# Kernel optimization log

Measured on AMD Instinct MI355X. Metric: run time of the kernel, lower is better.

Reference implementation:

```python
import jax, jax.numpy as jnp
import numpy as np

N_LOC = 20000
N_EXP = 200000
H = 64
E = 1500000
L = 400000


def setup_inputs() -> dict:
    key = jax.random.key(0)
    ks = jax.random.split(key, 24)
    f = jnp.float32
    w = lambda k, shp: jax.random.normal(k, shp, dtype=f) * 0.1
    # edges: ('location','of','experts'): src in [0,N_LOC), dst in [0,N_EXP)
    src = jax.random.randint(ks[0], (E,), 0, N_LOC)
    dst = jax.random.randint(ks[1], (E,), 0, N_EXP)
    edge_of = jnp.stack([src, dst])          # location -> experts
    edge_rev = jnp.stack([dst, src])         # experts -> location (ToUndirected)
    row = jax.random.randint(ks[2], (L,), 0, N_LOC)
    col = jax.random.randint(ks[3], (L,), 0, N_EXP)
    edge_label_index = jnp.stack([row, col])
    return dict(
        emb_loc=w(ks[4], (N_LOC, H)), emb_exp=w(ks[5], (N_EXP, H)),
        W1l_of=w(ks[6], (H, H)), b1_of=jnp.zeros((H,), f), W1r_of=w(ks[7], (H, H)),
        W1l_rev=w(ks[8], (H, H)), b1_rev=jnp.zeros((H,), f), W1r_rev=w(ks[9], (H, H)),
        W2l_of=w(ks[10], (H, H)), b2_of=jnp.zeros((H,), f), W2r_of=w(ks[11], (H, H)),
        W2l_rev=w(ks[12], (H, H)), b2_rev=jnp.zeros((H,), f), W2r_rev=w(ks[13], (H, H)),
        dW1=w(ks[14], (2 * H, H)), db1=jnp.zeros((H,), f),
        dW2=w(ks[15], (H, 1)), db2=jnp.zeros((1,), f),
        edge_of=edge_of, edge_rev=edge_rev, edge_label_index=edge_label_index,
    )


def _sage(x_src, x_dst, edge, Wl, b, Wr, n_dst):
    # PyG SAGEConv: lin_l(mean of neighbor msgs) + lin_r(x_dst); bias only in lin_l
    s, d = edge[0], edge[1]
    msg = x_src[s]                                   # [E, H] gather
    summed = jax.ops.segment_sum(msg, d, num_segments=n_dst)
    cnt = jax.ops.segment_sum(jnp.ones((edge.shape[1],), x_src.dtype), d, num_segments=n_dst)
    agg = summed / jnp.maximum(cnt, 1.0)[:, None]
    return agg @ Wl + b + x_dst @ Wr


def reference(emb_loc, emb_exp,
              W1l_of, b1_of, W1r_of, W1l_rev, b1_rev, W1r_rev,
              W2l_of, b2_of, W2r_of, W2l_rev, b2_rev, W2r_rev,
              dW1, db1, dW2, db2,
              edge_of, edge_rev, edge_label_index):
    # layer 1 (to_hetero: one conv per edge type; each dst type has one incoming type)
    z_exp = jax.nn.relu(_sage(emb_loc, emb_exp, edge_of, W1l_of, b1_of, W1r_of, N_EXP))
    z_loc = jax.nn.relu(_sage(emb_exp, emb_loc, edge_rev, W1l_rev, b1_rev, W1r_rev, N_LOC))
    # layer 2 (no relu)
    z_exp2 = _sage(z_loc, z_exp, edge_of, W2l_of, b2_of, W2r_of, N_EXP)
    z_loc2 = _sage(z_exp, z_loc, edge_rev, W2l_rev, b2_rev, W2r_rev, N_LOC)
    # EdgeDecoder: gather-concat-MLP
    row, col = edge_label_index[0], edge_label_index[1]
    z = jnp.concatenate([z_loc2[row], z_exp2[col]], axis=-1)  # [L, 2H]
    h = jax.nn.relu(z @ dW1 + db1)
    out = (h @ dW2 + db2).reshape(-1)
    return out
```

## Files before the change

### kernel.cpp

```cpp
#include <hip/hip_runtime.h>

#define H 64
#define NE 1500000
#define NLOC 20000
#define NEXP 200000
#define NL 400000
#define PAD_E 32
#define PAD_L 128
#define EPT 8
#define FILL_CHUNK 2048

#define WS_NEED 90480000ULL

typedef int vint4 __attribute__((ext_vector_type(4)));
typedef _Float16 f16x8 __attribute__((ext_vector_type(8)));
typedef float f32x4 __attribute__((ext_vector_type(4)));

__device__ __forceinline__ float bcastf(float v, int k) {
  return __int_as_float(__builtin_amdgcn_readlane(__float_as_int(v), k));
}
__device__ __forceinline__ int bcasti(int v, int k) {
  return __builtin_amdgcn_readlane(v, k);
}

__global__ __launch_bounds__(256) void fill_kernel(
    const int* __restrict__ src, const int* __restrict__ dst,
    int* __restrict__ cnt_loc, int* __restrict__ cnt_exp,
    int* __restrict__ nbr_loc, unsigned short* __restrict__ nbr_exp)
{
  const int p = blockIdx.x & 7;
  const int chunk = blockIdx.x >> 3;
  const long base = (long)chunk * FILL_CHUNK + threadIdx.x * EPT;
  if (base >= NE) return;
  vint4 s0 = *(const vint4*)(src + base);
  vint4 s1 = *(const vint4*)(src + base + 4);
  vint4 d0 = *(const vint4*)(dst + base);
  vint4 d1 = *(const vint4*)(dst + base + 4);
  int ss[EPT] = {s0.x, s0.y, s0.z, s0.w, s1.x, s1.y, s1.z, s1.w};
  int dd[EPT] = {d0.x, d0.y, d0.z, d0.w, d1.x, d1.y, d1.z, d1.w};
  const int elo = p * (NEXP / 8), ehi = elo + NEXP / 8;
  const int llo = p * (NLOC / 8), lhi = llo + NLOC / 8;
#pragma unroll
  for (int k = 0; k < EPT; k++) {
    const int d = dd[k];
    if (d >= elo && d < ehi) {
      int pos = atomicAdd(&cnt_exp[d], 1);
      if (pos < PAD_E) nbr_exp[d * PAD_E + pos] = (unsigned short)ss[k];
    }
  }
#pragma unroll
  for (int k = 0; k < EPT; k++) {
    const int s = ss[k];
    if (s >= llo && s < lhi) {
      int pos = atomicAdd(&cnt_loc[s], 1);
      if (pos < PAD_L) nbr_loc[s * PAD_L + pos] = dd[k];
    }
  }
}

__global__ __launch_bounds__(256, 4) void dense_linear_kernel(
    const float* __restrict__ x, _Float16* __restrict__ out16,
    float* __restrict__ out32, const float* __restrict__ W, int n)
{
  const int lane = threadIdx.x & 63;
  const int gw = (blockIdx.x * 256 + threadIdx.x) >> 6;
  const int nw = (gridDim.x * 256) >> 6;
  float w[H];
#pragma unroll
  for (int k = 0; k < H; k++) w[k] = W[k * H + lane];
  for (int i = gw; i < n; i += nw) {
    const float xv = x[i * H + lane];
    float a0 = 0.f, a1 = 0.f;
#pragma unroll
    for (int k = 0; k < H; k += 2) {
      a0 += bcastf(xv, k)     * w[k];
      a1 += bcastf(xv, k + 1) * w[k + 1];
    }
    if (out16) out16[i * H + lane] = (_Float16)(a0 + a1);
    else       out32[i * H + lane] = a0 + a1;
  }
}

__global__ __launch_bounds__(256, 4) void mfma_pass_kernel(
    const unsigned short* __restrict__ nbr, const int* __restrict__ cnt,
    const _Float16* __restrict__ y,
    const float* a32, const _Float16* a16,
    _Float16* out1, const float* __restrict__ W1,
    const float* __restrict__ bias, int relu,
    _Float16* out2, const float* __restrict__ W2)
{
  const int w = threadIdx.x >> 6;
  const int lane = threadIdx.x & 63;
  const int q = lane >> 4;
  const int cidx = lane & 15;
  const int rb = blockIdx.x * 16;

  __shared__ float Gs[16 * H];

  f16x8 b1lo, b1hi, b2lo, b2hi;
#pragma unroll
  for (int j = 0; j < 8; j++) {
    b1lo[j] = (_Float16)W1[(q * 8 + j) * H + w * 16 + cidx];
    b1hi[j] = (_Float16)W1[(32 + q * 8 + j) * H + w * 16 + cidx];
  }
  if (out2) {
#pragma unroll
    for (int j = 0; j < 8; j++) {
      b2lo[j] = (_Float16)W2[(q * 8 + j) * H + w * 16 + cidx];
      b2hi[j] = (_Float16)W2[(32 + q * 8 + j) * H + w * 16 + cidx];
    }
  }

  if (y) {
    for (int rr = 0; rr < 4; rr++) {
      const int i = rb + w * 4 + rr;
      const int c = cnt[i];
      const int cc = min(c, PAD_E);
      const unsigned short* nb = nbr + (long)i * PAD_E;
      float s0 = 0.f, s1 = 0.f, s2 = 0.f, s3 = 0.f;
      const int id = (lane < cc) ? (int)nb[lane] : 0;
      int k = 0;
      const int m4 = cc & ~3;
      for (; k < m4; k += 4) {
        const int i0 = bcasti(id, k), i1 = bcasti(id, k + 1),
                  i2 = bcasti(id, k + 2), i3 = bcasti(id, k + 3);
        s0 += (float)y[(long)i0 * H + lane];
        s1 += (float)y[(long)i1 * H + lane];
        s2 += (float)y[(long)i2 * H + lane];
        s3 += (float)y[(long)i3 * H + lane];
      }
      for (; k < cc; k++) s0 += (float)y[(long)bcasti(id, k) * H + lane];
      Gs[(w * 4 + rr) * H + lane] =
          ((s0 + s1) + (s2 + s3)) / fmaxf((float)c, 1.0f);
    }
  }

  f16x8 a0, a1;
  if (a16) {
    const _Float16* ar = a16 + (long)(rb + cidx) * H;
    a0 = *(const f16x8*)(ar + q * 8);
    a1 = *(const f16x8*)(ar + 32 + q * 8);
  } else {
    const float* ar = a32 + (long)(rb + cidx) * H;
#pragma unroll
    for (int j = 0; j < 8; j++) {
      a0[j] = (_Float16)ar[q * 8 + j];
      a1[j] = (_Float16)ar[32 + q * 8 + j];
    }
  }
  f32x4 acc1 = {0.f, 0.f, 0.f, 0.f};
  acc1 = __builtin_amdgcn_mfma_f32_16x16x32_f16(a0, b1lo, acc1, 0, 0, 0);
  acc1 = __builtin_amdgcn_mfma_f32_16x16x32_f16(a1, b1hi, acc1, 0, 0, 0);
  f32x4 acc2 = {0.f, 0.f, 0.f, 0.f};
  if (out2) {
    acc2 = __builtin_amdgcn_mfma_f32_16x16x32_f16(a0, b2lo, acc2, 0, 0, 0);
    acc2 = __builtin_amdgcn_mfma_f32_16x16x32_f16(a1, b2hi, acc2, 0, 0, 0);
  }

  const float bj = bias ? bias[w * 16 + cidx] : 0.f;
  __syncthreads();
#pragma unroll
  for (int reg = 0; reg < 4; reg++) {
    const int r = q * 4 + reg;
    float v = acc1[reg] + bj;
    if (y) v += Gs[r * H + w * 16 + cidx];
    if (relu) v = fmaxf(v, 0.f);
    out1[(long)(rb + r) * H + w * 16 + cidx] = (_Float16)v;
    if (out2)
      out2[(long)(rb + r) * H + w * 16 + cidx] = (_Float16)acc2[reg];
  }
}

__global__ __launch_bounds__(256, 4) void loc_gather_kernel(
    const int* __restrict__ nbr, const int* __restrict__ cnt,
    const _Float16* __restrict__ T, const float* __restrict__ x,
    float* __restrict__ out, const float* __restrict__ Wr,
    const float* __restrict__ bias, int n, int relu)
{
  const int lane = threadIdx.x & 63;
  const int gw = (blockIdx.x * 256 + threadIdx.x) >> 6;
  const int nw = (gridDim.x * 256) >> 6;
  float wr[H];
#pragma unroll
  for (int k = 0; k < H; k++) wr[k] = Wr[k * H + lane];
  const float bj = bias[lane];
  for (int i = gw; i < n; i += nw) {
    const int c = cnt[i];
    const int cc = min(c, PAD_L);
    const int* nb = nbr + (long)i * PAD_L;
    float s0 = 0.f, s1 = 0.f, s2 = 0.f, s3 = 0.f;
    int e = 0;
    while (e < cc) {
      const int m = min(cc - e, 64);
      const int id = (lane < m) ? nb[e + lane] : 0;
      int k = 0;
      const int m4 = m & ~3;
      for (; k < m4; k += 4) {
        const int i0 = bcasti(id, k), i1 = bcasti(id, k + 1),
                  i2 = bcasti(id, k + 2), i3 = bcasti(id, k + 3);
        s0 += (float)T[(long)i0 * H + lane];
        s1 += (float)T[(long)i1 * H + lane];
        s2 += (float)T[(long)i2 * H + lane];
        s3 += (float)T[(long)i3 * H + lane];
      }
      for (; k < m; k++) s0 += (float)T[(long)bcasti(id, k) * H + lane];
      e += m;
    }
    const float agg = ((s0 + s1) + (s2 + s3)) / fmaxf((float)c, 1.0f);
    const float xv = x[i * H + lane];
    float a0 = 0.f, a1 = 0.f;
#pragma unroll
    for (int k = 0; k < H; k += 2) {
      a0 += bcastf(xv, k)     * wr[k];
      a1 += bcastf(xv, k + 1) * wr[k + 1];
    }
    float acc = agg + bj + a0 + a1;
    if (relu) acc = fmaxf(acc, 0.0f);
    out[i * H + lane] = acc;
  }
}

__global__ __launch_bounds__(256, 4) void edge_kernel(
    const int* __restrict__ row, const int* __restrict__ col,
    const float* __restrict__ P, const _Float16* __restrict__ Q,
    const float* __restrict__ db1, const float* __restrict__ dW2,
    const float* __restrict__ db2, float* __restrict__ out)
{
  const int lane = threadIdx.x & 63;
  const int gw = (blockIdx.x * 256 + threadIdx.x) >> 6;
  const int nw = (gridDim.x * 256) >> 6;
  const float bj = db1[lane];
  const float w2 = dW2[lane];
  const float b2 = db2[0];
  for (int e = gw * 2; e < NL; e += nw * 2) {
    const int r0 = row[e],     c0 = col[e];
    const int r1 = row[e + 1], c1 = col[e + 1];
    const float p0 = P[(long)r0 * H + lane];
    const float q0 = (float)Q[(long)c0 * H + lane];
    const float p1 = P[(long)r1 * H + lane];
    const float q1 = (float)Q[(long)c1 * H + lane];
    float h0 = fmaxf(p0 + q0 + bj, 0.0f) * w2;
    float h1 = fmaxf(p1 + q1 + bj, 0.0f) * w2;
#pragma unroll
    for (int off = 1; off < 64; off <<= 1) {
      h0 += __shfl_xor(h0, off);
      h1 += __shfl_xor(h1, off);
    }
    if (lane == 0) {
      out[e]     = h0 + b2;
      out[e + 1] = h1 + b2;
    }
  }
}

extern "C" void kernel_launch(void* const* d_in, const int* in_sizes, int n_in,
                              void* d_out, int out_size, void* d_ws, size_t ws_size,
                              hipStream_t stream) {
  const float* emb_loc = (const float*)d_in[0];
  const float* emb_exp = (const float*)d_in[1];
  const float* W1l_of  = (const float*)d_in[2];
  const float* b1_of   = (const float*)d_in[3];
  const float* W1r_of  = (const float*)d_in[4];
  const float* W1l_rev = (const float*)d_in[5];
  const float* b1_rev  = (const float*)d_in[6];
  const float* W1r_rev = (const float*)d_in[7];
  const float* W2l_of  = (const float*)d_in[8];
  const float* b2_of   = (const float*)d_in[9];
  const float* W2r_of  = (const float*)d_in[10];
  const float* W2l_rev = (const float*)d_in[11];
  const float* b2_rev  = (const float*)d_in[12];
  const float* W2r_rev = (const float*)d_in[13];
  const float* dW1     = (const float*)d_in[14];
  const float* db1     = (const float*)d_in[15];
  const float* dW2     = (const float*)d_in[16];
  const float* db2     = (const float*)d_in[17];
  const int*   edge_of = (const int*)d_in[18];
  const int*   eli     = (const int*)d_in[20];

  const int* src = edge_of;
  const int* dst = edge_of + NE;
  const int* row = eli;
  const int* col = eli + NL;

  if (ws_size < WS_NEED) return;

  char* ws = (char*)d_ws;
  int*            cnt_loc = (int*)(ws);
  int*            cnt_exp = (int*)(ws + 80000);
  int*            nbr_loc = (int*)(ws + 880000);
  unsigned short* nbr_exp = (unsigned short*)(ws + 11120000);
  _Float16*       Ylh     = (_Float16*)(ws + 23920000);
  _Float16*       Y2lh    = (_Float16*)(ws + 26480000);
  float*          z_loc   = (float*)(ws + 29040000);
  float*          z_loc2  = (float*)(ws + 34160000);
  _Float16*       ZE      = (_Float16*)(ws + 39280000);
  _Float16*       TH      = (_Float16*)(ws + 64880000);
  float*          out     = (float*)d_out;

  (void)hipMemsetAsync(ws, 0, 880000, stream);
  const int chunks = (NE + FILL_CHUNK - 1) / FILL_CHUNK;
  fill_kernel<<<chunks * 8, 256, 0, stream>>>(src, dst, cnt_loc, cnt_exp,
                                              nbr_loc, nbr_exp);

  dense_linear_kernel<<<1280, 256, 0, stream>>>(emb_loc, Ylh, nullptr,
                                                W1l_of, NLOC);
  mfma_pass_kernel<<<NEXP / 16, 256, 0, stream>>>(nbr_exp, cnt_exp, Ylh,
      emb_exp, (const _Float16*)nullptr, ZE, W1r_of, b1_of, 1, TH, W1l_rev);
  loc_gather_kernel<<<1250, 256, 0, stream>>>(nbr_loc, cnt_loc, TH,
      emb_loc, z_loc, W1r_rev, b1_rev, NLOC, 1);

  dense_linear_kernel<<<1280, 256, 0, stream>>>(z_loc, Y2lh, nullptr,
                                                W2l_of, NLOC);
  mfma_pass_kernel<<<NEXP / 16, 256, 0, stream>>>(nbr_exp, cnt_exp, Y2lh,
      (const float*)nullptr, ZE, ZE, W2r_of, b2_of, 0, TH, W2l_rev);
  loc_gather_kernel<<<1250, 256, 0, stream>>>(nbr_loc, cnt_loc, TH,
      z_loc, z_loc2, W2r_rev, b2_rev, NLOC, 0);

  dense_linear_kernel<<<1280, 256, 0, stream>>>(z_loc2, nullptr, z_loc2,
                                                dW1, NLOC);
  mfma_pass_kernel<<<NEXP / 16, 256, 0, stream>>>(nbr_exp, cnt_exp,
      (const _Float16*)nullptr, (const float*)nullptr, ZE, ZE, dW1 + H * H,
      (const float*)nullptr, 0, (_Float16*)nullptr, (const float*)nullptr);
  edge_kernel<<<2048, 256, 0, stream>>>(row, col, z_loc2, ZE,
                                        db1, dW2, db2, out);
}
```

Measured before the change: 616.0 us.

## Fold decoder weights into layer-2 convs and make fill XCC-local with work queue

Precomputes products of the layer-2 SAGE weights with the two halves of the decoder's first weight matrix, so layer 2 directly emits decoder-projected features. This removes one dense linear pass and one full MFMA pass over the expert nodes. The fill kernel now reads its partition from the hardware XCC id, pulls chunks from a per-partition atomic queue, and uses workgroup-scope atomics with nontemporal loads. That keeps each partition's atomics on a single XCC, but workgroup-scope atomics are only correct if every block that touches a partition really runs on the same XCC, and fp16 rounding now occurs after the folded products.

```diff
diff --git a/kernel.cpp b/kernel.cpp
--- a/kernel.cpp
+++ b/kernel.cpp
@@ -9,8 +9,11 @@
 #define PAD_L 128
 #define EPT 8
 #define FILL_CHUNK 2048
-
-#define WS_NEED 90480000ULL
+#define NCHUNK ((NE + FILL_CHUNK - 1) / FILL_CHUNK)
+
+#define XCC_GETREG_IMM ((20) | ((0) << 6) | ((4 - 1) << 11))
+
+#define WS_NEED 90546112ULL
 
 typedef int vint4 __attribute__((ext_vector_type(4)));
 typedef _Float16 f16x8 __attribute__((ext_vector_type(8)));
@@ -22,45 +25,105 @@
 __device__ __forceinline__ int bcasti(int v, int k) {
   return __builtin_amdgcn_readlane(v, k);
 }
+__device__ __forceinline__ int atomLocal(int* p, int v) {
+  return __hip_atomic_fetch_add(p, v, __ATOMIC_RELAXED, __HIP_MEMORY_SCOPE_WORKGROUP);
+}
 
 __global__ __launch_bounds__(256) void fill_kernel(
     const int* __restrict__ src, const int* __restrict__ dst,
     int* __restrict__ cnt_loc, int* __restrict__ cnt_exp,
-    int* __restrict__ nbr_loc, unsigned short* __restrict__ nbr_exp)
-{
-  const int p = blockIdx.x & 7;
-  const int chunk = blockIdx.x >> 3;
-  const long base = (long)chunk * FILL_CHUNK + threadIdx.x * EPT;
-  if (base >= NE) return;
-  vint4 s0 = *(const vint4*)(src + base);
-  vint4 s1 = *(const vint4*)(src + base + 4);
-  vint4 d0 = *(const vint4*)(dst + base);
-  vint4 d1 = *(const vint4*)(dst + base + 4);
-  int ss[EPT] = {s0.x, s0.y, s0.z, s0.w, s1.x, s1.y, s1.z, s1.w};
-  int dd[EPT] = {d0.x, d0.y, d0.z, d0.w, d1.x, d1.y, d1.z, d1.w};
+    int* __restrict__ nbr_loc, unsigned short* __restrict__ nbr_exp,
+    int* __restrict__ qcur)
+{
+  const int p = __builtin_amdgcn_s_getreg(XCC_GETREG_IMM) & 7;
   const int elo = p * (NEXP / 8), ehi = elo + NEXP / 8;
   const int llo = p * (NLOC / 8), lhi = llo + NLOC / 8;
-#pragma unroll
-  for (int k = 0; k < EPT; k++) {
-    const int d = dd[k];
-    if (d >= elo && d < ehi) {
-      int pos = atomicAdd(&cnt_exp[d], 1);
-      if (pos < PAD_E) nbr_exp[d * PAD_E + pos] = (unsigned short)ss[k];
-    }
-  }
-#pragma unroll
-  for (int k = 0; k < EPT; k++) {
-    const int s = ss[k];
-    if (s >= llo && s < lhi) {
-      int pos = atomicAdd(&cnt_loc[s], 1);
-      if (pos < PAD_L) nbr_loc[s * PAD_L + pos] = dd[k];
-    }
+  __shared__ int chunk_s;
+  for (;;) {
+    __syncthreads();
+    if (threadIdx.x == 0) chunk_s = atomicAdd(&qcur[p], 1);
+    __syncthreads();
+    const int chunk = chunk_s;
+    if (chunk >= NCHUNK) return;
+    const long base = (long)chunk * FILL_CHUNK + threadIdx.x * EPT;
+    if (base >= NE) continue;
+    vint4 s0 = __builtin_nontemporal_load((const vint4*)(src + base));
+    vint4 s1 = __builtin_nontemporal_load((const vint4*)(src + base + 4));
+    vint4 d0 = __builtin_nontemporal_load((const vint4*)(dst + base));
+    vint4 d1 = __builtin_nontemporal_load((const vint4*)(dst + base + 4));
+    int ss[EPT] = {s0.x, s0.y, s0.z, s0.w, s1.x, s1.y, s1.z, s1.w};
+    int dd[EPT] = {d0.x, d0.y, d0.z, d0.w, d1.x, d1.y, d1.z, d1.w};
+#pragma unroll
+    for (int k = 0; k < EPT; k++) {
+      const int d = dd[k];
+      if (d >= elo && d < ehi) {
+        int pos = atomLocal(&cnt_exp[d], 1);
+        if (pos < PAD_E) nbr_exp[d * PAD_E + pos] = (unsigned short)ss[k];
+      }
+    }
+#pragma unroll
+    for (int k = 0; k < EPT; k++) {
+      const int s = ss[k];
+      if (s >= llo && s < lhi) {
+        int pos = atomLocal(&cnt_loc[s], 1);
+        if (pos < PAD_L) nbr_loc[s * PAD_L + pos] = dd[k];
+      }
+    }
+  }
+}
+
+__global__ __launch_bounds__(256) void fold_kernel(
+    const float* __restrict__ W2r_of, const float* __restrict__ W2l_of,
+    const float* __restrict__ W2l_rev, const float* __restrict__ W2r_rev,
+    const float* __restrict__ dW1, const float* __restrict__ b2_of,
+    const float* __restrict__ b2_rev,
+    float* __restrict__ Wf_q, float* __restrict__ Wf_y2,
+    float* __restrict__ Wf_t2, float* __restrict__ Wf_p,
+    float* __restrict__ bf_q, float* __restrict__ bf_p)
+{
+  const int lane = threadIdx.x & 63;
+  const int w = threadIdx.x >> 6;
+  const float* dW1a = dW1;
+  const float* dW1b = dW1 + H * H;
+  if (blockIdx.x < 4) {
+    const float* A; const float* B; float* C;
+    switch (blockIdx.x) {
+      case 0:  A = W2r_of;  B = dW1b; C = Wf_q;  break;
+      case 1:  A = W2l_of;  B = dW1b; C = Wf_y2; break;
+      case 2:  A = W2l_rev; B = dW1a; C = Wf_t2; break;
+      default: A = W2r_rev; B = dW1a; C = Wf_p;  break;
+    }
+    float b[H];
+#pragma unroll
+    for (int k = 0; k < H; k++) b[k] = B[k * H + lane];
+    for (int r = w * 16; r < w * 16 + 16; r++) {
+      const float xv = A[r * H + lane];
+      float a0 = 0.f, a1 = 0.f;
+#pragma unroll
+      for (int k = 0; k < H; k += 2) {
+        a0 += bcastf(xv, k)     * b[k];
+        a1 += bcastf(xv, k + 1) * b[k + 1];
+      }
+      C[r * H + lane] = a0 + a1;
+    }
+  } else if (w < 2) {
+    const float* bv_src = (w == 0) ? b2_of : b2_rev;
+    const float* B      = (w == 0) ? dW1b  : dW1a;
+    float* o            = (w == 0) ? bf_q  : bf_p;
+    float wk[H];
+#pragma unroll
+    for (int k = 0; k < H; k++) wk[k] = B[k * H + lane];
+    const float bv = bv_src[lane];
+    float a = 0.f;
+#pragma unroll
+    for (int k = 0; k < H; k++) a += bcastf(bv, k) * wk[k];
+    o[lane] = a;
   }
 }
 
 __global__ __launch_bounds__(256, 4) void dense_linear_kernel(
     const float* __restrict__ x, _Float16* __restrict__ out16,
-    float* __restrict__ out32, const float* __restrict__ W, int n)
+    const float* __restrict__ W, int n)
 {
   const int lane = threadIdx.x & 63;
   const int gw = (blockIdx.x * 256 + threadIdx.x) >> 6;
@@ -76,8 +139,7 @@
       a0 += bcastf(xv, k)     * w[k];
       a1 += bcastf(xv, k + 1) * w[k + 1];
     }
-    if (out16) out16[i * H + lane] = (_Float16)(a0 + a1);
-    else       out32[i * H + lane] = a0 + a1;
+    out16[i * H + lane] = (_Float16)(a0 + a1);
   }
 }
 
@@ -287,40 +349,42 @@
   char* ws = (char*)d_ws;
   int*            cnt_loc = (int*)(ws);
   int*            cnt_exp = (int*)(ws + 80000);
-  int*            nbr_loc = (int*)(ws + 880000);
-  unsigned short* nbr_exp = (unsigned short*)(ws + 11120000);
-  _Float16*       Ylh     = (_Float16*)(ws + 23920000);
-  _Float16*       Y2lh    = (_Float16*)(ws + 26480000);
-  float*          z_loc   = (float*)(ws + 29040000);
-  float*          z_loc2  = (float*)(ws + 34160000);
-  _Float16*       ZE      = (_Float16*)(ws + 39280000);
-  _Float16*       TH      = (_Float16*)(ws + 64880000);
+  int*            qcur    = (int*)(ws + 880000);
+  int*            nbr_loc = (int*)(ws + 880064);
+  unsigned short* nbr_exp = (unsigned short*)(ws + 11120064);
+  _Float16*       Ylh     = (_Float16*)(ws + 23920064);
+  _Float16*       Y2fh    = (_Float16*)(ws + 26480064);
+  float*          z_loc   = (float*)(ws + 29040064);
+  float*          P       = (float*)(ws + 34160064);
+  _Float16*       ZE      = (_Float16*)(ws + 39280064);
+  _Float16*       TH      = (_Float16*)(ws + 64880064);
+  float*          Wf_q    = (float*)(ws + 90480064);
+  float*          Wf_y2   = (float*)(ws + 90496448);
+  float*          Wf_t2   = (float*)(ws + 90512832);
+  float*          Wf_p    = (float*)(ws + 90529216);
+  float*          bf_q    = (float*)(ws + 90545600);
+  float*          bf_p    = (float*)(ws + 90545856);
   float*          out     = (float*)d_out;
 
-  (void)hipMemsetAsync(ws, 0, 880000, stream);
-  const int chunks = (NE + FILL_CHUNK - 1) / FILL_CHUNK;
-  fill_kernel<<<chunks * 8, 256, 0, stream>>>(src, dst, cnt_loc, cnt_exp,
-                                              nbr_loc, nbr_exp);
-
-  dense_linear_kernel<<<1280, 256, 0, stream>>>(emb_loc, Ylh, nullptr,
-                                                W1l_of, NLOC);
+  (void)hipMemsetAsync(ws, 0, 880064, stream);
+  fill_kernel<<<2048, 256, 0, stream>>>(src, dst, cnt_loc, cnt_exp,
+                                        nbr_loc, nbr_exp, qcur);
+  fold_kernel<<<5, 256, 0, stream>>>(W2r_of, W2l_of, W2l_rev, W2r_rev,
+                                     dW1, b2_of, b2_rev,
+                                     Wf_q, Wf_y2, Wf_t2, Wf_p, bf_q, bf_p);
+
+  dense_linear_kernel<<<1280, 256, 0, stream>>>(emb_loc, Ylh, W1l_of, NLOC);
   mfma_pass_kernel<<<NEXP / 16, 256, 0, stream>>>(nbr_exp, cnt_exp, Ylh,
       emb_exp, (const _Float16*)nullptr, ZE, W1r_of, b1_of, 1, TH, W1l_rev);
   loc_gather_kernel<<<1250, 256, 0, stream>>>(nbr_loc, cnt_loc, TH,
       emb_loc, z_loc, W1r_rev, b1_rev, NLOC, 1);
 
-  dense_linear_kernel<<<1280, 256, 0, stream>>>(z_loc, Y2lh, nullptr,
-                                                W2l_of, NLOC);
-  mfma_pass_kernel<<<NEXP / 16, 256, 0, stream>>>(nbr_exp, cnt_exp, Y2lh,
-      (const float*)nullptr, ZE, ZE, W2r_of, b2_of, 0, TH, W2l_rev);
+  dense_linear_kernel<<<1280, 256, 0, stream>>>(z_loc, Y2fh, Wf_y2, NLOC);
+  mfma_pass_kernel<<<NEXP / 16, 256, 0, stream>>>(nbr_exp, cnt_exp, Y2fh,
+      (const float*)nullptr, ZE, ZE, Wf_q, bf_q, 0, TH, Wf_t2);
   loc_gather_kernel<<<1250, 256, 0, stream>>>(nbr_loc, cnt_loc, TH,
-      z_loc, z_loc2, W2r_rev, b2_rev, NLOC, 0);
-
-  dense_linear_kernel<<<1280, 256, 0, stream>>>(z_loc2, nullptr, z_loc2,
-                                                dW1, NLOC);
-  mfma_pass_kernel<<<NEXP / 16, 256, 0, stream>>>(nbr_exp, cnt_exp,
-      (const _Float16*)nullptr, (const float*)nullptr, ZE, ZE, dW1 + H * H,
-      (const float*)nullptr, 0, (_Float16*)nullptr, (const float*)nullptr);
-  edge_kernel<<<2048, 256, 0, stream>>>(row, col, z_loc2, ZE,
+      z_loc, P, Wf_p, bf_p, NLOC, 0);
+
+  edge_kernel<<<2048, 256, 0, stream>>>(row, col, P, ZE,
                                         db1, dW2, db2, out);
 }
```

New measurement: 647.8 us. 5.2% more time.
